# Optimization experiments

Measured on AMD Instinct MI355X. Metric: run time of the kernel, lower is better.

Reference implementation:

```python
import jax, jax.numpy as jnp
import numpy as np

BS, TS, VOCAB, F = 8192, 100, 100000, 64

def _tri_idx(ts):
    # flat indices of strictly-upper-triangular entries of a ts x ts matrix
    i, j = np.triu_indices(ts, k=1)
    return jnp.asarray(i * ts + j)

def setup_inputs() -> dict:
    key = jax.random.key(0)
    ks = jax.random.split(key, 5)
    x = jax.random.randint(ks[0], (BS, TS), 0, VOCAB)
    emb = jax.random.normal(ks[1], (VOCAB, F), jnp.float32) * 0.02
    w_deep = jax.random.normal(ks[2], (F, F // 2), jnp.float32) * 0.05
    b_deep = jnp.zeros((F // 2,), jnp.float32)
    out_dim = TS * (TS - 1) // 2 + TS * (F // 2) + TS * F  # fm + deep + wide
    w_ffn = jax.random.normal(ks[3], (out_dim, 1), jnp.float32) * 0.01
    b_ffn = jnp.zeros((1,), jnp.float32)
    return {"x": x, "emb": emb, "w_deep": w_deep, "b_deep": b_deep,
            "w_ffn": w_ffn, "b_ffn": b_ffn}

def reference(x, emb, w_deep, b_deep, w_ffn, b_ffn):
    e = emb[x]                                  # [bs, ts, f]
    bs, ts, f = e.shape
    # pairwise dot products; keep only strictly-upper pairs (i<j)
    fm = jnp.einsum('btf,byf->bty', e, e)       # [bs, ts, ts]
    fm = fm.reshape(bs, ts * ts)[:, _tri_idx(ts)]   # [bs, ts*(ts-1)/2]
    deep = jax.nn.relu(e @ w_deep + b_deep).reshape(bs, -1)  # [bs, ts*f/2]
    wide = e.reshape(bs, ts * f)
    concat = jnp.concatenate([deep, fm, wide], axis=-1)
    return jax.nn.sigmoid(concat @ w_ffn + b_ffn)  # [bs, 1]
```

## Files before the change

kernel.cpp:

```cpp
#include <hip/hip_runtime.h>
#include <cmath>


#define TS 100
#define F  64
#define FD 32
#define RP 112
#define OFF_FM 3200
#define OFF_WIDE 8150
#define NFM_T 28
#define NUNITS 42
#define VOCAB 100000

typedef __attribute__((ext_vector_type(8))) short short8;
typedef __attribute__((ext_vector_type(4))) float f32x4;

__device__ __forceinline__ ushort f2bf(float x) {
    uint u = __float_as_uint(x);
    u = (u + 0x7FFFu + ((u >> 16) & 1u)) >> 16;
    return (ushort)u;
}
__device__ __forceinline__ float bf2f(ushort h) {
    return __uint_as_float((uint)h << 16);
}
__device__ __forceinline__ int triidx(int i, int j) {
    return i * (199 - i) / 2 + (j - i - 1);
}
__device__ __forceinline__ short8 ldfrag(const ushort* base, int row, int kbyte, int lane) {
    int col = (kbyte + ((lane >> 4) << 4)) ^ ((row & 7) << 4);
    return *reinterpret_cast<const short8*>(
        reinterpret_cast<const char*>(base) + row * 128 + col);
}

__global__ __launch_bounds__(256)
void emb_cvt(const float* __restrict__ src, ushort* __restrict__ dst, int n8) {
    int i = blockIdx.x * 256 + threadIdx.x;
    if (i >= n8) return;
    const float4* s = reinterpret_cast<const float4*>(src) + (size_t)i * 2;
    float4 a = s[0], b = s[1];
    ushort t[8] = { f2bf(a.x), f2bf(a.y), f2bf(a.z), f2bf(a.w),
                    f2bf(b.x), f2bf(b.y), f2bf(b.z), f2bf(b.w) };
    reinterpret_cast<uint4*>(dst)[i] = *reinterpret_cast<const uint4*>(t);
}

template<bool EMBBF>
__global__ __launch_bounds__(256)
void deepfm_mfma(const int* __restrict__ x,
                 const float* __restrict__ embf,
                 const ushort* __restrict__ embh,
                 const float* __restrict__ w_deep,
                 const float* __restrict__ b_deep,
                 const float* __restrict__ w_ffn,
                 const float* __restrict__ b_ffn,
                 float* __restrict__ out)
{
    __shared__ ushort e_lds[RP * F];
    __shared__ ushort wdT[FD * F];
    __shared__ int    xs[TS];
    __shared__ float  red[4];

    const int tid  = threadIdx.x;
    const int b    = blockIdx.x;
    const int lane = tid & 63;
    const int wave = tid >> 6;

    if (tid < TS) xs[tid] = x[(size_t)b * TS + tid];
    {
        int n = tid & 31, k8 = tid >> 5;
        ushort t[8];
        #pragma unroll
        for (int j = 0; j < 8; ++j) t[j] = f2bf(w_deep[(k8 * 8 + j) * FD + n]);
        int col = (k8 * 16) ^ ((n & 7) << 4);
        *reinterpret_cast<uint4*>(reinterpret_cast<char*>(wdT) + n * 128 + col)
            = *reinterpret_cast<const uint4*>(t);
    }
    __syncthreads();
    for (int j = tid; j < RP * 8; j += 256) {
        int r = j >> 3, k8 = j & 7;
        int col = (k8 * 16) ^ ((r & 7) << 4);
        char* dst = reinterpret_cast<char*>(e_lds) + r * 128 + col;
        if (r < TS) {
            if (EMBBF) {
                *reinterpret_cast<uint4*>(dst) =
                    *reinterpret_cast<const uint4*>(embh + (size_t)xs[r] * F + k8 * 8);
            } else {
                const float* s = embf + (size_t)xs[r] * F + k8 * 8;
                float4 a = reinterpret_cast<const float4*>(s)[0];
                float4 c = reinterpret_cast<const float4*>(s)[1];
                ushort t[8] = { f2bf(a.x), f2bf(a.y), f2bf(a.z), f2bf(a.w),
                                f2bf(c.x), f2bf(c.y), f2bf(c.z), f2bf(c.w) };
                *reinterpret_cast<uint4*>(dst) = *reinterpret_cast<const uint4*>(t);
            }
        } else {
            *reinterpret_cast<uint4*>(dst) = make_uint4(0, 0, 0, 0);
        }
    }
    __syncthreads();

    float z = 0.f;

    for (int u = wave; u < NUNITS; u += 4) {
        f32x4 acc = {0.f, 0.f, 0.f, 0.f};
        if (u < NFM_T) {
            int ti = 0, rem = u;
            while (rem >= 7 - ti) { rem -= 7 - ti; ++ti; }
            int tj = ti + rem;
            int ar = ti * 16 + (lane & 15), br = tj * 16 + (lane & 15);
            short8 a0 = ldfrag(e_lds, ar, 0, lane);
            short8 b0 = ldfrag(e_lds, br, 0, lane);
            short8 a1 = ldfrag(e_lds, ar, 64, lane);
            short8 b1 = ldfrag(e_lds, br, 64, lane);
            acc = __builtin_amdgcn_mfma_f32_16x16x32_bf16(a0, b0, acc, 0, 0, 0);
            acc = __builtin_amdgcn_mfma_f32_16x16x32_bf16(a1, b1, acc, 0, 0, 0);
            int jc = tj * 16 + (lane & 15);
            #pragma unroll
            for (int r = 0; r < 4; ++r) {
                int i = ti * 16 + ((lane >> 4) << 2) + r;
                if (i < jc && jc < TS)
                    z += acc[r] * w_ffn[OFF_FM + triidx(i, jc)];
            }
        } else {
            int v = u - NFM_T, tt = v >> 1, kt = v & 1;
            int ar = tt * 16 + (lane & 15), br = kt * 16 + (lane & 15);
            short8 a0 = ldfrag(e_lds, ar, 0, lane);
            short8 b0 = ldfrag(wdT, br, 0, lane);
            short8 a1 = ldfrag(e_lds, ar, 64, lane);
            short8 b1 = ldfrag(wdT, br, 64, lane);
            acc = __builtin_amdgcn_mfma_f32_16x16x32_bf16(a0, b0, acc, 0, 0, 0);
            acc = __builtin_amdgcn_mfma_f32_16x16x32_bf16(a1, b1, acc, 0, 0, 0);
            int k = kt * 16 + (lane & 15);
            float bk = b_deep[k];
            #pragma unroll
            for (int r = 0; r < 4; ++r) {
                int t = tt * 16 + ((lane >> 4) << 2) + r;
                if (t < TS) {
                    float d = acc[r] + bk;
                    z += fmaxf(d, 0.f) * w_ffn[t * FD + k];
                }
            }
        }
    }

    for (int j = tid; j < TS * 8; j += 256) {
        int t = j >> 3, k8 = j & 7;
        int col = (k8 * 16) ^ ((t & 7) << 4);
        short8 v = *reinterpret_cast<const short8*>(
            reinterpret_cast<const char*>(e_lds) + t * 128 + col);
        const float* w = w_ffn + OFF_WIDE + t * F + k8 * 8;
        #pragma unroll
        for (int q = 0; q < 8; ++q) z += bf2f((ushort)v[q]) * w[q];
    }

    #pragma unroll
    for (int off = 32; off > 0; off >>= 1) z += __shfl_down(z, off, 64);
    if ((tid & 63) == 0) red[wave] = z;
    __syncthreads();
    if (tid == 0) {
        float t = red[0] + red[1] + red[2] + red[3] + b_ffn[0];
        out[b] = 1.f / (1.f + expf(-t));
    }
}

extern "C" void kernel_launch(void* const* d_in, const int* in_sizes, int n_in,
                              void* d_out, int out_size, void* d_ws, size_t ws_size,
                              hipStream_t stream) {
    const int*   x      = (const int*)  d_in[0];
    const float* emb    = (const float*)d_in[1];
    const float* w_deep = (const float*)d_in[2];
    const float* b_deep = (const float*)d_in[3];
    const float* w_ffn  = (const float*)d_in[4];
    const float* b_ffn  = (const float*)d_in[5];
    float* out = (float*)d_out;
    const int bs = in_sizes[0] / TS;
    const size_t need = (size_t)VOCAB * F * sizeof(ushort);

    if (ws_size >= need) {
        ushort* embh = (ushort*)d_ws;
        const int n8 = VOCAB * F / 8;
        hipLaunchKernelGGL(emb_cvt, dim3((n8 + 255) / 256), dim3(256), 0, stream,
                           emb, embh, n8);
        hipLaunchKernelGGL((deepfm_mfma<true>), dim3(bs), dim3(256), 0, stream,
                           x, emb, embh, w_deep, b_deep, w_ffn, b_ffn, out);
    } else {
        hipLaunchKernelGGL((deepfm_mfma<false>), dim3(bs), dim3(256), 0, stream,
                           x, emb, (const ushort*)nullptr, w_deep, b_deep, w_ffn, b_ffn, out);
    }
}
```

Before: 155.0 us.

## Recast FM pairwise term as E^T·W_fm·E matmul with prebuilt symmetric weight

The FM term sum_{i<j} w_ij (e_i·e_j) is rewritten as sum over t,f of E[t,f]·(W_sym E)[t,f]. A prep kernel builds a symmetric, half-scaled bf16 weight matrix and a transposed bf16 w_deep. The main kernel transposes E into shared memory and computes the FM part with one GEMM per wave (B fragments loaded straight from global). The wide term is fused into that epilogue. This removes the scattered triangular w_ffn gathers and the 28-tile pairwise loop, at the cost of an extra prep launch, an LDS transpose, and bf16 rounding of the FM weights.

```diff
diff --git a/kernel.cpp b/kernel.cpp
--- a/kernel.cpp
+++ b/kernel.cpp
@@ -6,13 +6,15 @@
 #define F  64
 #define FD 32
 #define RP 112
+#define KP 128
 #define OFF_FM 3200
 #define OFF_WIDE 8150
-#define NFM_T 28
-#define NUNITS 42
 #define VOCAB 100000
+#define WFM_ELEMS (RP*KP)
+#define WDT_ELEMS (FD*F)
 
 typedef __attribute__((ext_vector_type(8))) short short8;
+typedef __attribute__((ext_vector_type(4))) short short4v;
 typedef __attribute__((ext_vector_type(4))) float f32x4;
 
 __device__ __forceinline__ ushort f2bf(float x) {
@@ -23,13 +25,16 @@
 __device__ __forceinline__ float bf2f(ushort h) {
     return __uint_as_float((uint)h << 16);
 }
-__device__ __forceinline__ int triidx(int i, int j) {
-    return i * (199 - i) / 2 + (j - i - 1);
-}
-__device__ __forceinline__ short8 ldfrag(const ushort* base, int row, int kbyte, int lane) {
-    int col = (kbyte + ((lane >> 4) << 4)) ^ ((row & 7) << 4);
+
+__device__ __forceinline__ short8 ldE(const ushort* base, int row, int kbyte, int lane) {
+    int off = (kbyte + ((lane >> 4) << 4)) ^ ((row & 7) << 4);
     return *reinterpret_cast<const short8*>(
-        reinterpret_cast<const char*>(base) + row * 128 + col);
+        reinterpret_cast<const char*>(base) + row * 128 + off);
+}
+__device__ __forceinline__ short8 ldET(const ushort* base, int row, int kbyte, int lane) {
+    int off = (kbyte + ((lane >> 4) << 4)) ^ ((row & 7) << 4);
+    return *reinterpret_cast<const short8*>(
+        reinterpret_cast<const char*>(base) + row * 256 + off);
 }
 
 __global__ __launch_bounds__(256)
@@ -43,19 +48,39 @@
     reinterpret_cast<uint4*>(dst)[i] = *reinterpret_cast<const uint4*>(t);
 }
 
+__global__ __launch_bounds__(256)
+void prep(const float* __restrict__ w_ffn, const float* __restrict__ w_deep,
+          ushort* __restrict__ wfm, ushort* __restrict__ wdt) {
+    int j = blockIdx.x * 256 + threadIdx.x;
+    if (j < WFM_ELEMS) {
+        int t = j >> 7, tp = j & 127;
+        ushort v = 0;
+        if (t < TS && tp < TS && t != tp) {
+            int i = min(t, tp), jj = max(t, tp);
+            v = f2bf(0.5f * w_ffn[OFF_FM + i * (199 - i) / 2 + (jj - i - 1)]);
+        }
+        wfm[j] = v;
+    } else if (j < WFM_ELEMS + WDT_ELEMS) {
+        int q = j - WFM_ELEMS;
+        int k = q >> 6, f = q & 63;
+        wdt[q] = f2bf(w_deep[f * FD + k]);
+    }
+}
+
 template<bool EMBBF>
-__global__ __launch_bounds__(256)
-void deepfm_mfma(const int* __restrict__ x,
+__global__ __launch_bounds__(256, 4)
+void deepfm_main(const int* __restrict__ x,
                  const float* __restrict__ embf,
                  const ushort* __restrict__ embh,
-                 const float* __restrict__ w_deep,
+                 const ushort* __restrict__ wfm,
+                 const ushort* __restrict__ wdt,
                  const float* __restrict__ b_deep,
                  const float* __restrict__ w_ffn,
                  const float* __restrict__ b_ffn,
                  float* __restrict__ out)
 {
-    __shared__ ushort e_lds[RP * F];
-    __shared__ ushort wdT[FD * F];
+    __shared__ ushort Es[RP * F];
+    __shared__ ushort ETs[F * KP];
     __shared__ int    xs[TS];
     __shared__ float  red[4];
 
@@ -63,22 +88,16 @@
     const int b    = blockIdx.x;
     const int lane = tid & 63;
     const int wave = tid >> 6;
+    const int lr   = lane & 15;
+    const int lg   = lane >> 4;
 
     if (tid < TS) xs[tid] = x[(size_t)b * TS + tid];
-    {
-        int n = tid & 31, k8 = tid >> 5;
-        ushort t[8];
-        #pragma unroll
-        for (int j = 0; j < 8; ++j) t[j] = f2bf(w_deep[(k8 * 8 + j) * FD + n]);
-        int col = (k8 * 16) ^ ((n & 7) << 4);
-        *reinterpret_cast<uint4*>(reinterpret_cast<char*>(wdT) + n * 128 + col)
-            = *reinterpret_cast<const uint4*>(t);
-    }
-    __syncthreads();
+    __syncthreads();
+
     for (int j = tid; j < RP * 8; j += 256) {
         int r = j >> 3, k8 = j & 7;
-        int col = (k8 * 16) ^ ((r & 7) << 4);
-        char* dst = reinterpret_cast<char*>(e_lds) + r * 128 + col;
+        int off = (k8 * 16) ^ ((r & 7) << 4);
+        char* dst = reinterpret_cast<char*>(Es) + r * 128 + off;
         if (r < TS) {
             if (EMBBF) {
                 *reinterpret_cast<uint4*>(dst) =
@@ -97,58 +116,82 @@
     }
     __syncthreads();
 
-    float z = 0.f;
-
-    for (int u = wave; u < NUNITS; u += 4) {
-        f32x4 acc = {0.f, 0.f, 0.f, 0.f};
-        if (u < NFM_T) {
-            int ti = 0, rem = u;
-            while (rem >= 7 - ti) { rem -= 7 - ti; ++ti; }
-            int tj = ti + rem;
-            int ar = ti * 16 + (lane & 15), br = tj * 16 + (lane & 15);
-            short8 a0 = ldfrag(e_lds, ar, 0, lane);
-            short8 b0 = ldfrag(e_lds, br, 0, lane);
-            short8 a1 = ldfrag(e_lds, ar, 64, lane);
-            short8 b1 = ldfrag(e_lds, br, 64, lane);
-            acc = __builtin_amdgcn_mfma_f32_16x16x32_bf16(a0, b0, acc, 0, 0, 0);
-            acc = __builtin_amdgcn_mfma_f32_16x16x32_bf16(a1, b1, acc, 0, 0, 0);
-            int jc = tj * 16 + (lane & 15);
+    {
+        int half = tid >> 7, r = tid & 127;
+        ushort vals[32];
+        if (r < RP) {
             #pragma unroll
-            for (int r = 0; r < 4; ++r) {
-                int i = ti * 16 + ((lane >> 4) << 2) + r;
-                if (i < jc && jc < TS)
-                    z += acc[r] * w_ffn[OFF_FM + triidx(i, jc)];
+            for (int c = 0; c < 4; ++c) {
+                int off = (half * 64 + c * 16) ^ ((r & 7) << 4);
+                *reinterpret_cast<short8*>(vals + c * 8) =
+                    *reinterpret_cast<const short8*>(
+                        reinterpret_cast<const char*>(Es) + r * 128 + off);
             }
         } else {
-            int v = u - NFM_T, tt = v >> 1, kt = v & 1;
-            int ar = tt * 16 + (lane & 15), br = kt * 16 + (lane & 15);
-            short8 a0 = ldfrag(e_lds, ar, 0, lane);
-            short8 b0 = ldfrag(wdT, br, 0, lane);
-            short8 a1 = ldfrag(e_lds, ar, 64, lane);
-            short8 b1 = ldfrag(wdT, br, 64, lane);
-            acc = __builtin_amdgcn_mfma_f32_16x16x32_bf16(a0, b0, acc, 0, 0, 0);
-            acc = __builtin_amdgcn_mfma_f32_16x16x32_bf16(a1, b1, acc, 0, 0, 0);
-            int k = kt * 16 + (lane & 15);
-            float bk = b_deep[k];
             #pragma unroll
-            for (int r = 0; r < 4; ++r) {
-                int t = tt * 16 + ((lane >> 4) << 2) + r;
-                if (t < TS) {
-                    float d = acc[r] + bk;
-                    z += fmaxf(d, 0.f) * w_ffn[t * FD + k];
-                }
+            for (int q = 0; q < 32; ++q) vals[q] = 0;
+        }
+        #pragma unroll
+        for (int q = 0; q < 32; ++q) {
+            int f = half * 32 + q;
+            int off = (r * 2) ^ ((f & 7) << 4);
+            *reinterpret_cast<ushort*>(reinterpret_cast<char*>(ETs) + f * 256 + off) = vals[q];
+        }
+    }
+    __syncthreads();
+
+    float z = 0.f;
+
+    short8 A0 = ldET(ETs, wave * 16 + lr, 0,   lane);
+    short8 A1 = ldET(ETs, wave * 16 + lr, 64,  lane);
+    short8 A2 = ldET(ETs, wave * 16 + lr, 128, lane);
+    short8 A3 = ldET(ETs, wave * 16 + lr, 192, lane);
+    const int f0 = wave * 16 + lg * 4;
+    for (int nt = 0; nt < 7; ++nt) {
+        f32x4 acc = {0.f, 0.f, 0.f, 0.f};
+        const ushort* bp = wfm + (nt * 16 + lr) * KP + lg * 8;
+        short8 B0 = *reinterpret_cast<const short8*>(bp);
+        short8 B1 = *reinterpret_cast<const short8*>(bp + 32);
+        short8 B2 = *reinterpret_cast<const short8*>(bp + 64);
+        short8 B3 = *reinterpret_cast<const short8*>(bp + 96);
+        acc = __builtin_amdgcn_mfma_f32_16x16x32_bf16(A0, B0, acc, 0, 0, 0);
+        acc = __builtin_amdgcn_mfma_f32_16x16x32_bf16(A1, B1, acc, 0, 0, 0);
+        acc = __builtin_amdgcn_mfma_f32_16x16x32_bf16(A2, B2, acc, 0, 0, 0);
+        acc = __builtin_amdgcn_mfma_f32_16x16x32_bf16(A3, B3, acc, 0, 0, 0);
+        int t = nt * 16 + lr;
+        int tc = min(t, TS - 1);
+        float4 ww = *reinterpret_cast<const float4*>(w_ffn + OFF_WIDE + tc * F + f0);
+        int evoff = (f0 * 2) ^ ((t & 7) << 4);
+        short4v ev = *reinterpret_cast<const short4v*>(
+            reinterpret_cast<const char*>(Es) + t * 128 + evoff);
+        #pragma unroll
+        for (int r2 = 0; r2 < 4; ++r2)
+            z += bf2f((ushort)ev[r2]) * (acc[r2] + (&ww.x)[r2]);
+    }
+
+    for (int nt = wave; nt < 7; nt += 4) {
+        int t = nt * 16 + lr;
+        int tc = min(t, TS - 1);
+        bool valid = t < TS;
+        short8 Bb0 = ldE(Es, t, 0,  lane);
+        short8 Bb1 = ldE(Es, t, 64, lane);
+        #pragma unroll
+        for (int m = 0; m < 2; ++m) {
+            f32x4 acc = {0.f, 0.f, 0.f, 0.f};
+            const ushort* ap = wdt + (m * 16 + lr) * F + lg * 8;
+            short8 Aa0 = *reinterpret_cast<const short8*>(ap);
+            short8 Aa1 = *reinterpret_cast<const short8*>(ap + 32);
+            acc = __builtin_amdgcn_mfma_f32_16x16x32_bf16(Aa0, Bb0, acc, 0, 0, 0);
+            acc = __builtin_amdgcn_mfma_f32_16x16x32_bf16(Aa1, Bb1, acc, 0, 0, 0);
+            int k0 = m * 16 + lg * 4;
+            float4 wd4 = *reinterpret_cast<const float4*>(w_ffn + tc * FD + k0);
+            float4 bd4 = *reinterpret_cast<const float4*>(b_deep + k0);
+            #pragma unroll
+            for (int r2 = 0; r2 < 4; ++r2) {
+                float w = valid ? (&wd4.x)[r2] : 0.f;
+                z += fmaxf(acc[r2] + (&bd4.x)[r2], 0.f) * w;
             }
         }
-    }
-
-    for (int j = tid; j < TS * 8; j += 256) {
-        int t = j >> 3, k8 = j & 7;
-        int col = (k8 * 16) ^ ((t & 7) << 4);
-        short8 v = *reinterpret_cast<const short8*>(
-            reinterpret_cast<const char*>(e_lds) + t * 128 + col);
-        const float* w = w_ffn + OFF_WIDE + t * F + k8 * 8;
-        #pragma unroll
-        for (int q = 0; q < 8; ++q) z += bf2f((ushort)v[q]) * w[q];
     }
 
     #pragma unroll
@@ -172,17 +215,26 @@
     const float* b_ffn  = (const float*)d_in[5];
     float* out = (float*)d_out;
     const int bs = in_sizes[0] / TS;
-    const size_t need = (size_t)VOCAB * F * sizeof(ushort);
-
-    if (ws_size >= need) {
+    const size_t embh_bytes = (size_t)VOCAB * F * 2;
+    const size_t w_bytes = (size_t)(WFM_ELEMS + WDT_ELEMS) * 2;
+
+    if (ws_size >= embh_bytes + w_bytes) {
         ushort* embh = (ushort*)d_ws;
+        ushort* wfm  = (ushort*)((char*)d_ws + embh_bytes);
+        ushort* wdt  = wfm + WFM_ELEMS;
         const int n8 = VOCAB * F / 8;
         hipLaunchKernelGGL(emb_cvt, dim3((n8 + 255) / 256), dim3(256), 0, stream,
                            emb, embh, n8);
-        hipLaunchKernelGGL((deepfm_mfma<true>), dim3(bs), dim3(256), 0, stream,
-                           x, emb, embh, w_deep, b_deep, w_ffn, b_ffn, out);
+        hipLaunchKernelGGL(prep, dim3(64), dim3(256), 0, stream,
+                           w_ffn, w_deep, wfm, wdt);
+        hipLaunchKernelGGL((deepfm_main<true>), dim3(bs), dim3(256), 0, stream,
+                           x, emb, embh, wfm, wdt, b_deep, w_ffn, b_ffn, out);
     } else {
-        hipLaunchKernelGGL((deepfm_mfma<false>), dim3(bs), dim3(256), 0, stream,
-                           x, emb, (const ushort*)nullptr, w_deep, b_deep, w_ffn, b_ffn, out);
-    }
-}
+        ushort* wfm = (ushort*)d_ws;
+        ushort* wdt = wfm + WFM_ELEMS;
+        hipLaunchKernelGGL(prep, dim3(64), dim3(256), 0, stream,
+                           w_ffn, w_deep, wfm, wdt);
+        hipLaunchKernelGGL((deepfm_main<false>), dim3(bs), dim3(256), 0, stream,
+                           x, emb, (const ushort*)nullptr, wfm, wdt, b_deep, w_ffn, b_ffn, out);
+    }
+}
```

Measured after the change: 254.5 us. 1.64x slower.

## Precompute dense padded FM/deep output-weight tiles and fully unroll per-wave MFMA units

Applied to the files above, without the earlier changes.

Adds a prep kernel that scatters the triangular FM weights and the deep output weights into dense zero-padded 112-wide matrices, plus a pre-transposed bf16 w_deep, all held in workspace. The main kernel then reads contiguous float4 weights per MFMA tile, with no triangular index math or bounds masks. Per-wave unit loops are compile-time unrolled through templated dispatch with constant tile tables. This adds an extra kernel launch and workspace use, and the fallback path now writes to the workspace without checking its size.

```diff
diff --git a/kernel.cpp b/kernel.cpp
--- a/kernel.cpp
+++ b/kernel.cpp
@@ -8,12 +8,16 @@
 #define RP 112
 #define OFF_FM 3200
 #define OFF_WIDE 8150
-#define NFM_T 28
-#define NUNITS 42
 #define VOCAB 100000
+#define W2_ELEMS (RP*RP)
+#define W3_ELEMS (FD*RP)
+#define WDT_ELEMS (FD*F)
 
 typedef __attribute__((ext_vector_type(8))) short short8;
 typedef __attribute__((ext_vector_type(4))) float f32x4;
+
+constexpr int FM_TI[28] = {0,0,0,0,0,0,0, 1,1,1,1,1,1, 2,2,2,2,2, 3,3,3,3, 4,4,4, 5,5, 6};
+constexpr int FM_TJ[28] = {0,1,2,3,4,5,6, 1,2,3,4,5,6, 2,3,4,5,6, 3,4,5,6, 4,5,6, 5,6, 6};
 
 __device__ __forceinline__ ushort f2bf(float x) {
     uint u = __float_as_uint(x);
@@ -22,14 +26,6 @@
 }
 __device__ __forceinline__ float bf2f(ushort h) {
     return __uint_as_float((uint)h << 16);
-}
-__device__ __forceinline__ int triidx(int i, int j) {
-    return i * (199 - i) / 2 + (j - i - 1);
-}
-__device__ __forceinline__ short8 ldfrag(const ushort* base, int row, int kbyte, int lane) {
-    int col = (kbyte + ((lane >> 4) << 4)) ^ ((row & 7) << 4);
-    return *reinterpret_cast<const short8*>(
-        reinterpret_cast<const char*>(base) + row * 128 + col);
 }
 
 __global__ __launch_bounds__(256)
@@ -43,19 +39,79 @@
     reinterpret_cast<uint4*>(dst)[i] = *reinterpret_cast<const uint4*>(t);
 }
 
+__global__ __launch_bounds__(256)
+void prep(const float* __restrict__ w_ffn, const float* __restrict__ w_deep,
+          float* __restrict__ W2, float* __restrict__ W3, ushort* __restrict__ wdt) {
+    int j = blockIdx.x * 256 + threadIdx.x;
+    if (j < W2_ELEMS) {
+        int jc = j / RP, i = j % RP;
+        float v = 0.f;
+        if (i < jc && jc < TS)
+            v = w_ffn[OFF_FM + i * (199 - i) / 2 + (jc - i - 1)];
+        W2[j] = v;
+    } else if (j < W2_ELEMS + W3_ELEMS) {
+        int q = j - W2_ELEMS;
+        int k = q / RP, t = q % RP;
+        W3[q] = (t < TS) ? w_ffn[t * FD + k] : 0.f;
+    } else if (j < W2_ELEMS + W3_ELEMS + WDT_ELEMS) {
+        int q = j - W2_ELEMS - W3_ELEMS;
+        int k = q >> 6, f = q & 63;
+        wdt[q] = f2bf(w_deep[f * FD + k]);
+    }
+}
+
+template<int W>
+__device__ __forceinline__ float units(const char* esp, const char* wdp,
+                                       int c0, int c1,
+                                       const float* pW2, const float* pW3,
+                                       const float* bdl) {
+    float z = 0.f;
+    #pragma unroll
+    for (int u = W; u < 42; u += 4) {
+        f32x4 acc = {0.f, 0.f, 0.f, 0.f};
+        if (u < 28) {
+            const int ti = FM_TI[u], tj = FM_TJ[u];
+            short8 a0 = *reinterpret_cast<const short8*>(esp + ti * 2048 + c0);
+            short8 a1 = *reinterpret_cast<const short8*>(esp + ti * 2048 + c1);
+            short8 b0 = *reinterpret_cast<const short8*>(esp + tj * 2048 + c0);
+            short8 b1 = *reinterpret_cast<const short8*>(esp + tj * 2048 + c1);
+            acc = __builtin_amdgcn_mfma_f32_16x16x32_bf16(a0, b0, acc, 0, 0, 0);
+            acc = __builtin_amdgcn_mfma_f32_16x16x32_bf16(a1, b1, acc, 0, 0, 0);
+            float4 w = *reinterpret_cast<const float4*>(pW2 + tj * 1792 + ti * 16);
+            z += acc[0] * w.x + acc[1] * w.y + acc[2] * w.z + acc[3] * w.w;
+        } else {
+            const int v = u - 28, tt = v >> 1, kt = v & 1;
+            short8 a0 = *reinterpret_cast<const short8*>(esp + tt * 2048 + c0);
+            short8 a1 = *reinterpret_cast<const short8*>(esp + tt * 2048 + c1);
+            short8 b0 = *reinterpret_cast<const short8*>(wdp + kt * 2048 + c0);
+            short8 b1 = *reinterpret_cast<const short8*>(wdp + kt * 2048 + c1);
+            acc = __builtin_amdgcn_mfma_f32_16x16x32_bf16(a0, b0, acc, 0, 0, 0);
+            acc = __builtin_amdgcn_mfma_f32_16x16x32_bf16(a1, b1, acc, 0, 0, 0);
+            float bk = bdl[kt * 16];
+            float4 w = *reinterpret_cast<const float4*>(pW3 + kt * 1792 + tt * 16);
+            z += fmaxf(acc[0] + bk, 0.f) * w.x + fmaxf(acc[1] + bk, 0.f) * w.y
+               + fmaxf(acc[2] + bk, 0.f) * w.z + fmaxf(acc[3] + bk, 0.f) * w.w;
+        }
+    }
+    return z;
+}
+
 template<bool EMBBF>
 __global__ __launch_bounds__(256)
-void deepfm_mfma(const int* __restrict__ x,
+void deepfm_main(const int* __restrict__ x,
                  const float* __restrict__ embf,
                  const ushort* __restrict__ embh,
-                 const float* __restrict__ w_deep,
+                 const float* __restrict__ W2,
+                 const float* __restrict__ W3,
+                 const ushort* __restrict__ wdt,
                  const float* __restrict__ b_deep,
                  const float* __restrict__ w_ffn,
                  const float* __restrict__ b_ffn,
                  float* __restrict__ out)
 {
-    __shared__ ushort e_lds[RP * F];
+    __shared__ ushort Es[RP * F];
     __shared__ ushort wdT[FD * F];
+    __shared__ float  bdeep_lds[FD];
     __shared__ int    xs[TS];
     __shared__ float  red[4];
 
@@ -63,22 +119,23 @@
     const int b    = blockIdx.x;
     const int lane = tid & 63;
     const int wave = tid >> 6;
+    const int lr   = lane & 15;
+    const int lg   = lane >> 4;
 
     if (tid < TS) xs[tid] = x[(size_t)b * TS + tid];
+    if (tid < FD) bdeep_lds[tid] = b_deep[tid];
     {
-        int n = tid & 31, k8 = tid >> 5;
-        ushort t[8];
-        #pragma unroll
-        for (int j = 0; j < 8; ++j) t[j] = f2bf(w_deep[(k8 * 8 + j) * FD + n]);
-        int col = (k8 * 16) ^ ((n & 7) << 4);
-        *reinterpret_cast<uint4*>(reinterpret_cast<char*>(wdT) + n * 128 + col)
-            = *reinterpret_cast<const uint4*>(t);
+        int k = tid >> 3, k8 = tid & 7;
+        int col = (k8 * 16) ^ ((k & 7) << 4);
+        *reinterpret_cast<uint4*>(reinterpret_cast<char*>(wdT) + k * 128 + col)
+            = *reinterpret_cast<const uint4*>(wdt + k * F + k8 * 8);
     }
     __syncthreads();
+
     for (int j = tid; j < RP * 8; j += 256) {
         int r = j >> 3, k8 = j & 7;
         int col = (k8 * 16) ^ ((r & 7) << 4);
-        char* dst = reinterpret_cast<char*>(e_lds) + r * 128 + col;
+        char* dst = reinterpret_cast<char*>(Es) + r * 128 + col;
         if (r < TS) {
             if (EMBBF) {
                 *reinterpret_cast<uint4*>(dst) =
@@ -97,58 +154,34 @@
     }
     __syncthreads();
 
-    float z = 0.f;
-
-    for (int u = wave; u < NUNITS; u += 4) {
-        f32x4 acc = {0.f, 0.f, 0.f, 0.f};
-        if (u < NFM_T) {
-            int ti = 0, rem = u;
-            while (rem >= 7 - ti) { rem -= 7 - ti; ++ti; }
-            int tj = ti + rem;
-            int ar = ti * 16 + (lane & 15), br = tj * 16 + (lane & 15);
-            short8 a0 = ldfrag(e_lds, ar, 0, lane);
-            short8 b0 = ldfrag(e_lds, br, 0, lane);
-            short8 a1 = ldfrag(e_lds, ar, 64, lane);
-            short8 b1 = ldfrag(e_lds, br, 64, lane);
-            acc = __builtin_amdgcn_mfma_f32_16x16x32_bf16(a0, b0, acc, 0, 0, 0);
-            acc = __builtin_amdgcn_mfma_f32_16x16x32_bf16(a1, b1, acc, 0, 0, 0);
-            int jc = tj * 16 + (lane & 15);
-            #pragma unroll
-            for (int r = 0; r < 4; ++r) {
-                int i = ti * 16 + ((lane >> 4) << 2) + r;
-                if (i < jc && jc < TS)
-                    z += acc[r] * w_ffn[OFF_FM + triidx(i, jc)];
-            }
-        } else {
-            int v = u - NFM_T, tt = v >> 1, kt = v & 1;
-            int ar = tt * 16 + (lane & 15), br = kt * 16 + (lane & 15);
-            short8 a0 = ldfrag(e_lds, ar, 0, lane);
-            short8 b0 = ldfrag(wdT, br, 0, lane);
-            short8 a1 = ldfrag(e_lds, ar, 64, lane);
-            short8 b1 = ldfrag(wdT, br, 64, lane);
-            acc = __builtin_amdgcn_mfma_f32_16x16x32_bf16(a0, b0, acc, 0, 0, 0);
-            acc = __builtin_amdgcn_mfma_f32_16x16x32_bf16(a1, b1, acc, 0, 0, 0);
-            int k = kt * 16 + (lane & 15);
-            float bk = b_deep[k];
-            #pragma unroll
-            for (int r = 0; r < 4; ++r) {
-                int t = tt * 16 + ((lane >> 4) << 2) + r;
-                if (t < TS) {
-                    float d = acc[r] + bk;
-                    z += fmaxf(d, 0.f) * w_ffn[t * FD + k];
-                }
-            }
-        }
+    const int sw = (lr & 7) << 4;
+    const int c0 = (lg * 16) ^ sw;
+    const int c1 = (64 + lg * 16) ^ sw;
+    const char* esp = reinterpret_cast<const char*>(Es) + lr * 128;
+    const char* wdp = reinterpret_cast<const char*>(wdT) + lr * 128;
+    const float* pW2 = W2 + lr * RP + lg * 4;
+    const float* pW3 = W3 + lr * RP + lg * 4;
+    const float* bdl = bdeep_lds + lr;
+
+    float z;
+    switch (wave) {
+        case 0:  z = units<0>(esp, wdp, c0, c1, pW2, pW3, bdl); break;
+        case 1:  z = units<1>(esp, wdp, c0, c1, pW2, pW3, bdl); break;
+        case 2:  z = units<2>(esp, wdp, c0, c1, pW2, pW3, bdl); break;
+        default: z = units<3>(esp, wdp, c0, c1, pW2, pW3, bdl); break;
     }
 
     for (int j = tid; j < TS * 8; j += 256) {
         int t = j >> 3, k8 = j & 7;
-        int col = (k8 * 16) ^ ((t & 7) << 4);
+        int off = (k8 * 16) ^ ((t & 7) << 4);
         short8 v = *reinterpret_cast<const short8*>(
-            reinterpret_cast<const char*>(e_lds) + t * 128 + col);
-        const float* w = w_ffn + OFF_WIDE + t * F + k8 * 8;
-        #pragma unroll
-        for (int q = 0; q < 8; ++q) z += bf2f((ushort)v[q]) * w[q];
+            reinterpret_cast<const char*>(Es) + t * 128 + off);
+        const float2* w = reinterpret_cast<const float2*>(w_ffn + OFF_WIDE + t * F + k8 * 8);
+        float2 wa = w[0], wb = w[1], wc = w[2], wd = w[3];
+        z += bf2f((ushort)v[0]) * wa.x + bf2f((ushort)v[1]) * wa.y
+           + bf2f((ushort)v[2]) * wb.x + bf2f((ushort)v[3]) * wb.y
+           + bf2f((ushort)v[4]) * wc.x + bf2f((ushort)v[5]) * wc.y
+           + bf2f((ushort)v[6]) * wd.x + bf2f((ushort)v[7]) * wd.y;
     }
 
     #pragma unroll
@@ -172,17 +205,33 @@
     const float* b_ffn  = (const float*)d_in[5];
     float* out = (float*)d_out;
     const int bs = in_sizes[0] / TS;
-    const size_t need = (size_t)VOCAB * F * sizeof(ushort);
-
-    if (ws_size >= need) {
-        ushort* embh = (ushort*)d_ws;
+    const size_t embh_bytes = (size_t)VOCAB * F * 2;
+    const size_t w2_bytes = W2_ELEMS * 4;
+    const size_t w3_bytes = W3_ELEMS * 4;
+    const size_t wdt_bytes = WDT_ELEMS * 2;
+    const size_t wtot = w2_bytes + w3_bytes + wdt_bytes;
+    const int prep_jobs = W2_ELEMS + W3_ELEMS + WDT_ELEMS;
+
+    if (ws_size >= embh_bytes + wtot) {
+        ushort* embhp = (ushort*)d_ws;
+        float*  W2p   = (float*)((char*)d_ws + embh_bytes);
+        float*  W3p   = (float*)((char*)d_ws + embh_bytes + w2_bytes);
+        ushort* wdtp  = (ushort*)((char*)d_ws + embh_bytes + w2_bytes + w3_bytes);
         const int n8 = VOCAB * F / 8;
         hipLaunchKernelGGL(emb_cvt, dim3((n8 + 255) / 256), dim3(256), 0, stream,
-                           emb, embh, n8);
-        hipLaunchKernelGGL((deepfm_mfma<true>), dim3(bs), dim3(256), 0, stream,
-                           x, emb, embh, w_deep, b_deep, w_ffn, b_ffn, out);
+                           emb, embhp, n8);
+        hipLaunchKernelGGL(prep, dim3((prep_jobs + 255) / 256), dim3(256), 0, stream,
+                           w_ffn, w_deep, W2p, W3p, wdtp);
+        hipLaunchKernelGGL((deepfm_main<true>), dim3(bs), dim3(256), 0, stream,
+                           x, emb, embhp, W2p, W3p, wdtp, b_deep, w_ffn, b_ffn, out);
     } else {
-        hipLaunchKernelGGL((deepfm_mfma<false>), dim3(bs), dim3(256), 0, stream,
-                           x, emb, (const ushort*)nullptr, w_deep, b_deep, w_ffn, b_ffn, out);
-    }
-}
+        float*  W2p  = (float*)d_ws;
+        float*  W3p  = (float*)((char*)d_ws + w2_bytes);
+        ushort* wdtp = (ushort*)((char*)d_ws + w2_bytes + w3_bytes);
+        hipLaunchKernelGGL(prep, dim3((prep_jobs + 255) / 256), dim3(256), 0, stream,
+                           w_ffn, w_deep, W2p, W3p, wdtp);
+        hipLaunchKernelGGL((deepfm_main<false>), dim3(bs), dim3(256), 0, stream,
+                           x, emb, (const ushort*)nullptr, W2p, W3p, wdtp,
+                           b_deep, w_ffn, b_ffn, out);
+    }
+}
```

Result: slower. 158.9 us (+2.5%).
